# Performance work log

Measured on AMD Instinct MI355X. Metric: run time of the kernel, lower is better.

Reference implementation:

```python
import jax, jax.numpy as jnp
import numpy as np
from jax import lax

EPS = 1e-5  # BatchNorm eps (torch default)

def _up2_bilinear_ac(x):
    # bilinear upsample x2, align_corners=True; x: [B,C,H,W]
    B, C, H, W = x.shape
    def axis_interp(n_in, n_out):
        pos = jnp.arange(n_out, dtype=jnp.float32) * ((n_in - 1) / (n_out - 1))
        i0 = jnp.floor(pos).astype(jnp.int32)
        i1 = jnp.minimum(i0 + 1, n_in - 1)
        w = (pos - i0.astype(jnp.float32)).astype(x.dtype)
        return i0, i1, w
    i0, i1, wh = axis_interp(H, 2 * H)
    x = x[:, :, i0, :] * (1.0 - wh)[None, None, :, None] + x[:, :, i1, :] * wh[None, None, :, None]
    j0, j1, ww = axis_interp(W, 2 * W)
    x = x[:, :, :, j0] * (1.0 - ww) + x[:, :, :, j1] * ww
    return x

def setup_inputs() -> dict:
    key = jax.random.key(0)
    ks = jax.random.split(key, 8)
    B, Cin, Cout, H, W = 8, 64, 32, 128, 128
    att, K = 16, 2  # attention_channel = max(int(64*0.0625),16)=16; kernel_num=2
    n = lambda k, s, sc: jax.random.normal(k, s, jnp.float32) * sc
    return {
        'x': n(ks[0], (B, Cin, H, W), 1.0),
        'fc_w': n(ks[1], (att, Cin), 0.1),
        'bn_a_gamma': jnp.ones((att,), jnp.float32), 'bn_a_beta': jnp.zeros((att,), jnp.float32),
        'bn_a_mean': jnp.zeros((att,), jnp.float32), 'bn_a_var': jnp.ones((att,), jnp.float32),
        'ch_w': n(ks[2], (Cin, att), 0.1), 'ch_b': jnp.zeros((Cin,), jnp.float32),
        'fil_w': n(ks[3], (Cout, att), 0.1), 'fil_b': jnp.zeros((Cout,), jnp.float32),
        'sp_w': n(ks[4], (9, att), 0.1), 'sp_b': jnp.zeros((9,), jnp.float32),
        'k_w': n(ks[5], (K, att), 0.1), 'k_b': jnp.zeros((K,), jnp.float32),
        'weight': n(ks[6], (K, Cout, Cin, 3, 3), 0.05),
        'bn_gamma': jnp.ones((Cout,), jnp.float32), 'bn_beta': jnp.zeros((Cout,), jnp.float32),
        'bn_mean': jnp.zeros((Cout,), jnp.float32), 'bn_var': jnp.ones((Cout,), jnp.float32),
    }

def reference(x, fc_w, bn_a_gamma, bn_a_beta, bn_a_mean, bn_a_var,
              ch_w, ch_b, fil_w, fil_b, sp_w, sp_b, k_w, k_b,
              weight, bn_gamma, bn_beta, bn_mean, bn_var):
    x = _up2_bilinear_ac(x)
    B, Cin, H, W = x.shape
    K, Cout = weight.shape[0], weight.shape[1]
    # --- ODConv attention branch (on GAP features) ---
    g = x.mean(axis=(2, 3))                                    # [B,Cin]
    h = g @ fc_w.T                                             # [B,att]
    h = (h - bn_a_mean) / jnp.sqrt(bn_a_var + EPS) * bn_a_gamma + bn_a_beta
    h = jax.nn.relu(h)
    ch_att = jax.nn.sigmoid(h @ ch_w.T + ch_b)                 # [B,Cin]
    fil_att = jax.nn.sigmoid(h @ fil_w.T + fil_b)              # [B,Cout]
    sp_att = jax.nn.sigmoid(h @ sp_w.T + sp_b).reshape(B, 1, 1, 1, 3, 3)
    k_att = jax.nn.softmax(h @ k_w.T + k_b, axis=1).reshape(B, K, 1, 1, 1, 1)
    # per-sample aggregated filters: [B,Cout,Cin,3,3]
    agg_w = jnp.sum(k_att * sp_att * weight[None], axis=1)
    # --- dynamic conv (per-sample filter), channel-attended input ---
    x = x * ch_att[:, :, None, None]
    def conv1(xi, wi):
        return lax.conv_general_dilated(xi[None], wi, (1, 1), [(1, 1), (1, 1)],
                                        dimension_numbers=('NCHW', 'OIHW', 'NCHW'))[0]
    y = jax.vmap(conv1)(x, agg_w)                              # [B,Cout,H,W]
    y = y * fil_att[:, :, None, None]
    # --- BatchNorm2d (inference) + GELU (exact erf) ---
    y = (y - bn_mean[:, None, None]) / jnp.sqrt(bn_var[:, None, None] + EPS)
    y = y * bn_gamma[:, None, None] + bn_beta[:, None, None]
    return jax.nn.gelu(y, approximate=False)
```

## Files before the change

kernel.cpp:

```cpp
#include <hip/hip_runtime.h>
#include <hip/hip_bf16.h>

#define EPSBN 1e-5f

typedef short short8 __attribute__((ext_vector_type(8)));
typedef float f32x16 __attribute__((ext_vector_type(16)));

static __device__ __forceinline__ unsigned short f2u(float f){
  __hip_bfloat16 h = __float2bfloat16(f);
  union { __hip_bfloat16 h; unsigned short u; } c; c.h = h; return c.u;
}

#define WS_G     2048
#define WS_S     7168
#define WS_T     8192
#define WS_AGGB  16384
#define WS_XUP   327680

__global__ __launch_bounds__(256) void k_gap(const float* __restrict__ x, float* __restrict__ g){
  __shared__ float w[128];
  __shared__ float partial[4];
  int tid = threadIdx.x;
  if (tid < 128){
    int i = tid;
    float s = 0.f;
    int rstart = max(0, (int)floorf((float)(i-1)*(255.0f/127.0f)));
    #pragma unroll
    for (int k = 0; k < 8; ++k){
      int r = rstart + k;
      if (r <= 255){
        float pos = (float)r * (127.0f/255.0f);
        int i0 = (int)pos; float fr = pos - (float)i0; int i1 = min(i0+1,127);
        if (i0 == i) s += 1.0f - fr;
        if (i1 == i) s += fr;
      }
    }
    w[i] = s;
  }
  __syncthreads();
  const float4* xp = (const float4*)(x + ((size_t)blockIdx.x << 14));
  float s = 0.f;
  for (int gi = tid; gi < 4096; gi += 256){
    int i = gi >> 5, j4 = (gi & 31) * 4;
    float4 v = xp[gi];
    s += (v.x*w[j4] + v.y*w[j4+1] + v.z*w[j4+2] + v.w*w[j4+3]) * w[i];
  }
  for (int off = 32; off > 0; off >>= 1) s += __shfl_down(s, off, 64);
  if ((tid & 63) == 0) partial[tid >> 6] = s;
  __syncthreads();
  if (tid == 0) g[blockIdx.x] = (partial[0]+partial[1]+partial[2]+partial[3]) * (1.0f/65536.0f);
}

__global__ __launch_bounds__(256) void k_aggw(const float* __restrict__ g,
                      const float* __restrict__ fc_w,
                      const float* __restrict__ bga, const float* __restrict__ bba,
                      const float* __restrict__ bma, const float* __restrict__ bva,
                      const float* __restrict__ ch_w, const float* __restrict__ ch_b,
                      const float* __restrict__ fil_w, const float* __restrict__ fil_b,
                      const float* __restrict__ sp_w, const float* __restrict__ sp_b,
                      const float* __restrict__ k_w, const float* __restrict__ k_b,
                      const float* __restrict__ bn_g, const float* __restrict__ bn_b,
                      const float* __restrict__ bn_m, const float* __restrict__ bn_v,
                      const float* __restrict__ weight,
                      unsigned short* __restrict__ aggb,
                      float* __restrict__ sS, float* __restrict__ tT)
{
  __shared__ float h[8][16];
  int tid = threadIdx.x;
  if (tid < 128){
    int b = tid >> 4, a = tid & 15;
    float acc = 0.f;
    for (int c = 0; c < 64; ++c) acc += g[b*64+c] * fc_w[a*64+c];
    float v = (acc - bma[a]) * rsqrtf(bva[a] + EPSBN) * bga[a] + bba[a];
    h[b][a] = fmaxf(v, 0.f);
  }
  __syncthreads();

  int idx = blockIdx.x*256 + tid;
  int ci_l = idx & 31;
  int o    = (idx >> 5) & 31;
  int s    = (idx >> 10) % 9;
  int t2   = (idx >> 10) / 9;
  int cc   = t2 & 1, b = t2 >> 1;
  int ci   = cc*32 + ci_l;

  const float* hb = h[b];
  float zc = ch_b[ci], zs = sp_b[s];
  float z0 = k_b[0],  z1 = k_b[1];
  #pragma unroll
  for (int a = 0; a < 16; ++a){
    float hv = hb[a];
    zc += hv*ch_w[ci*16+a];
    zs += hv*sp_w[s*16+a];
    z0 += hv*k_w[a];
    z1 += hv*k_w[16+a];
  }
  float chv = 1.f/(1.f+expf(-zc));
  float spv = 1.f/(1.f+expf(-zs));
  float m = fmaxf(z0,z1);
  float e0 = expf(z0-m), e1 = expf(z1-m), inv = 1.f/(e0+e1);
  float ka0 = e0*inv, ka1 = e1*inv;
  float w0 = weight[(o*64+ci)*9+s];
  float w1 = weight[((32+o)*64+ci)*9+s];
  aggb[idx] = f2u(chv*spv*(ka0*w0 + ka1*w1));

  if (blockIdx.x == 0){
    int bb = tid >> 5, oo = tid & 31;
    float z = fil_b[oo];
    #pragma unroll
    for (int a = 0; a < 16; ++a) z += h[bb][a]*fil_w[oo*16+a];
    float f = 1.f/(1.f+expf(-z));
    float invs = rsqrtf(bn_v[oo] + EPSBN);
    sS[tid] = f * bn_g[oo] * invs;
    if (bb == 0) tT[oo] = bn_b[oo] - bn_m[oo]*bn_g[oo]*invs;
  }
}

__global__ __launch_bounds__(256) void k_up(const float* __restrict__ x,
                                            unsigned int* __restrict__ xup32)
{
  __shared__ float xin[16*798];
  int tid = threadIdx.x;
  int bi  = blockIdx.x;
  int strip = bi & 31, h16 = (bi >> 5) & 3, b = bi >> 7;
  int r0 = strip * 8;
  int i0b = (int)((float)r0 * (127.0f/255.0f));

  for (int e = tid; e < 12288; e += 256){
    int ir = e >> 11, rem = e & 2047, ci = rem >> 7, j = rem & 127;
    int row = min(i0b + ir, 127);
    xin[ci*798 + ir*133 + j] = x[(((size_t)(b*64 + h16*16 + ci)) << 14) + (row << 7) + j];
  }
  __syncthreads();

  int ci2 = tid & 7, cbase = tid >> 3;
  int j0t[8], j1t[8]; float wwt[8];
  #pragma unroll
  for (int jj = 0; jj < 8; ++jj){
    int c = cbase + 32*jj;
    float pos = (float)c * (127.0f/255.0f);
    int j0 = (int)pos;
    j0t[jj] = j0; j1t[jj] = min(j0+1,127); wwt[jj] = pos - (float)j0;
  }
  const float* base0 = &xin[(ci2*2+0)*798];
  const float* base1 = &xin[(ci2*2+1)*798];
  size_t plane32 = ((size_t)(b*4 + h16)) << 19;

  for (int rr = 0; rr < 8; ++rr){
    int r = r0 + rr;
    float posr = (float)r * (127.0f/255.0f);
    int i0 = (int)posr; float wh = posr - (float)i0;
    int ir0 = (i0 - i0b)*133, ir1 = (min(i0+1,127) - i0b)*133;
    #pragma unroll
    for (int jj = 0; jj < 8; ++jj){
      int c = cbase + 32*jj;
      int j0 = j0t[jj], j1 = j1t[jj]; float ww = wwt[jj];
      float v00 = base0[ir0+j0], v01 = base0[ir0+j1];
      float v10 = base0[ir1+j0], v11 = base0[ir1+j1];
      float a0 = v00 + (v01-v00)*ww;
      float a1 = v10 + (v11-v10)*ww;
      float r0v = a0 + (a1-a0)*wh;
      float u00 = base1[ir0+j0], u01 = base1[ir0+j1];
      float u10 = base1[ir1+j0], u11 = base1[ir1+j1];
      float b0 = u00 + (u01-u00)*ww;
      float b1 = u10 + (u11-u10)*ww;
      float r1v = b0 + (b1-b0)*wh;
      unsigned pack = (unsigned)f2u(r0v) | (((unsigned)f2u(r1v)) << 16);
      xup32[plane32 + (size_t)(r*256 + c)*8 + ci2] = pack;
    }
  }
}

#define XT_STRIDE 40
__global__ __launch_bounds__(256) void k_conv(const unsigned short* __restrict__ xup,
                                              const unsigned short* __restrict__ aggb,
                                              const float* __restrict__ sS,
                                              const float* __restrict__ tT,
                                              float* __restrict__ out)
{
  __shared__ unsigned short xt[18*18*XT_STRIDE];
  __shared__ float sSs[32], tTs[32];

  int tid = threadIdx.x;
  int bi  = blockIdx.x;
  int b   = bi >> 8, t = bi & 255;
  int p0  = (t >> 4) * 16, q0 = (t & 15) * 16;
  int lane = tid & 63, wv = tid >> 6;
  if (tid < 32){ sSs[tid] = sS[b*32+tid]; tTs[tid] = tT[tid]; }

  int ldsoff[6], pmoff[6]; bool val[6];
  int cnt = (tid < 16) ? 6 : 5;
  for (int k = 0; k < cnt; ++k){
    int e = tid + (k << 8);
    int rr = e / 72; int rem = e - rr*72;
    int qq = rem >> 2; int k2 = (rem >> 1) & 1; int kq = rem & 1;
    int gr = p0 - 1 + rr, gq = q0 - 1 + qq;
    val[k]    = ((unsigned)gr < 256u) && ((unsigned)gq < 256u);
    ldsoff[k] = (rr*18+qq)*XT_STRIDE + k2*16 + kq*8;
    pmoff[k]  = (k2 << 20) + (gr*256+gq)*16 + kq*8;
  }

  f32x16 acc[2];
  #pragma unroll
  for (int i = 0; i < 16; ++i){ acc[0][i] = 0.f; acc[1][i] = 0.f; }

  int n  = lane & 31;
  int kq = lane >> 5;

  for (int cc = 0; cc < 2; ++cc){
    if (cc) __syncthreads();
    const unsigned short* xb = xup + (((size_t)(b*4 + 2*cc)) << 20);
    for (int k = 0; k < cnt; ++k){
      short8 v = {0,0,0,0,0,0,0,0};
      if (val[k]) v = *(const short8*)&xb[pmoff[k]];
      *(short8*)&xt[ldsoff[k]] = v;
    }
    __syncthreads();

    const unsigned short* ab = aggb + (((size_t)(b*2+cc))*9*32 + n)*32 + kq*8;

    #pragma unroll
    for (int s = 0; s < 9; ++s){
      const int ky = s / 3, kx = s % 3;
      const unsigned short* ap = ab + s*1024;
      short8 av0 = *(const short8*)&ap[0];
      short8 av1 = *(const short8*)&ap[16];
      #pragma unroll
      for (int tt = 0; tt < 2; ++tt){
        int lr = 2*(2*wv + tt) + (n >> 4);
        int rr = lr + ky;
        int qq = (n & 15) + kx;
        const unsigned short* xrow = &xt[(rr*18+qq)*XT_STRIDE + kq*8];
        short8 bv0 = *(const short8*)&xrow[0];
        short8 bv1 = *(const short8*)&xrow[16];
        acc[tt] = __builtin_amdgcn_mfma_f32_32x32x16_bf16(av0, bv0, acc[tt], 0, 0, 0);
        acc[tt] = __builtin_amdgcn_mfma_f32_32x32x16_bf16(av1, bv1, acc[tt], 0, 0, 0);
      }
    }
  }

  #pragma unroll
  for (int tt = 0; tt < 2; ++tt){
    int lr = 2*(2*wv + tt) + (n >> 4);
    int p = p0 + lr, q = q0 + (n & 15);
    #pragma unroll
    for (int r = 0; r < 16; ++r){
      int o = (r & 3) + 8*(r >> 2) + 4*kq;
      float valv = acc[tt][r]*sSs[o] + tTs[o];
      float gl  = 0.5f*valv*(1.f + erff(valv*0.70710678118f));
      out[(((size_t)(b*32+o)) << 16) + (p << 8) + q] = gl;
    }
  }
}

extern "C" void kernel_launch(void* const* d_in, const int* in_sizes, int n_in,
                              void* d_out, int out_size, void* d_ws, size_t ws_size,
                              hipStream_t stream)
{
  const float* x     = (const float*)d_in[0];
  const float* fc_w  = (const float*)d_in[1];
  const float* bga   = (const float*)d_in[2];
  const float* bba   = (const float*)d_in[3];
  const float* bma   = (const float*)d_in[4];
  const float* bva   = (const float*)d_in[5];
  const float* ch_w  = (const float*)d_in[6];
  const float* ch_b  = (const float*)d_in[7];
  const float* fil_w = (const float*)d_in[8];
  const float* fil_b = (const float*)d_in[9];
  const float* sp_w  = (const float*)d_in[10];
  const float* sp_b  = (const float*)d_in[11];
  const float* k_w   = (const float*)d_in[12];
  const float* k_b   = (const float*)d_in[13];
  const float* weight= (const float*)d_in[14];
  const float* bn_g  = (const float*)d_in[15];
  const float* bn_b  = (const float*)d_in[16];
  const float* bn_m  = (const float*)d_in[17];
  const float* bn_v  = (const float*)d_in[18];

  char* ws = (char*)d_ws;
  float* g   = (float*)(ws + WS_G);
  float* sS  = (float*)(ws + WS_S);
  float* tT  = (float*)(ws + WS_T);
  unsigned short* aggb = (unsigned short*)(ws + WS_AGGB);
  unsigned short* xup  = (unsigned short*)(ws + WS_XUP);
  float* out = (float*)d_out;

  hipLaunchKernelGGL(k_gap,  dim3(512),  dim3(256), 0, stream, x, g);
  hipLaunchKernelGGL(k_aggw, dim3(576),  dim3(256), 0, stream, g, fc_w, bga, bba, bma, bva,
                     ch_w, ch_b, fil_w, fil_b, sp_w, sp_b, k_w, k_b,
                     bn_g, bn_b, bn_m, bn_v, weight, aggb, sS, tT);
  hipLaunchKernelGGL(k_up,   dim3(1024), dim3(256), 0, stream, x, (unsigned int*)xup);
  hipLaunchKernelGGL(k_conv, dim3(2048), dim3(256), 0, stream, xup, aggb, sS, tT, out);
}
```

Baseline: 201.3 us.

## Fuse GAP into upsample kernel and prefetch second channel chunk in conv

The global-average-pool reduction moves into the upsample kernel: each block reuses its staged input rows to compute partial weighted sums and adds them into g with atomics, after a memset. This removes a separate full read of x and one kernel launch. The conv kernel now prefetches the second channel-half tile into registers while the first half computes, and software-pipelines the weight fragment loads across filter taps. The cost is atomic float accumulation, which makes summation order nondeterministic, plus higher register pressure.

Result: faster. 191.0 us (-5.1%).

```diff
diff --git a/kernel.cpp b/kernel.cpp
--- a/kernel.cpp
+++ b/kernel.cpp
@@ -17,10 +17,18 @@
 #define WS_AGGB  16384
 #define WS_XUP   327680
 
-__global__ __launch_bounds__(256) void k_gap(const float* __restrict__ x, float* __restrict__ g){
+__global__ __launch_bounds__(256) void k_up(const float* __restrict__ x,
+                                            unsigned int* __restrict__ xup32,
+                                            float* __restrict__ g)
+{
+  __shared__ float xin[16*798];
   __shared__ float w[128];
-  __shared__ float partial[4];
   int tid = threadIdx.x;
+  int bi  = blockIdx.x;
+  int strip = bi & 31, h16 = (bi >> 5) & 3, b = bi >> 7;
+  int r0 = strip * 8;
+  int i0b = (int)((float)r0 * (127.0f/255.0f));
+
   if (tid < 128){
     int i = tid;
     float s = 0.f;
@@ -37,18 +45,70 @@
     }
     w[i] = s;
   }
-  __syncthreads();
-  const float4* xp = (const float4*)(x + ((size_t)blockIdx.x << 14));
-  float s = 0.f;
-  for (int gi = tid; gi < 4096; gi += 256){
-    int i = gi >> 5, j4 = (gi & 31) * 4;
-    float4 v = xp[gi];
-    s += (v.x*w[j4] + v.y*w[j4+1] + v.z*w[j4+2] + v.w*w[j4+3]) * w[i];
-  }
-  for (int off = 32; off > 0; off >>= 1) s += __shfl_down(s, off, 64);
-  if ((tid & 63) == 0) partial[tid >> 6] = s;
-  __syncthreads();
-  if (tid == 0) g[blockIdx.x] = (partial[0]+partial[1]+partial[2]+partial[3]) * (1.0f/65536.0f);
+  for (int e = tid; e < 12288; e += 256){
+    int ir = e >> 11, rem = e & 2047, ci = rem >> 7, j = rem & 127;
+    int row = min(i0b + ir, 127);
+    xin[ci*798 + ir*133 + j] = x[(((size_t)(b*64 + h16*16 + ci)) << 14) + (row << 7) + j];
+  }
+  __syncthreads();
+
+  {
+    int ci_l = tid >> 4, kk = tid & 15;
+    float s = 0.f;
+    const float* base = &xin[ci_l*798];
+    #pragma unroll
+    for (int row = 0; row < 4; ++row){
+      int grow = 4*strip + row;
+      int ir = grow - i0b;
+      const float* rp = base + ir*133 + kk*8;
+      float ss = 0.f;
+      #pragma unroll
+      for (int j = 0; j < 8; ++j) ss += rp[j]*w[kk*8+j];
+      s += w[grow]*ss;
+    }
+    s += __shfl_down(s, 8, 16);
+    s += __shfl_down(s, 4, 16);
+    s += __shfl_down(s, 2, 16);
+    s += __shfl_down(s, 1, 16);
+    if (kk == 0) atomicAdd(&g[b*64 + h16*16 + ci_l], s*(1.0f/65536.0f));
+  }
+
+  int ci2 = tid & 7, cbase = tid >> 3;
+  int j0t[8], j1t[8]; float wwt[8];
+  #pragma unroll
+  for (int jj = 0; jj < 8; ++jj){
+    int c = cbase + 32*jj;
+    float pos = (float)c * (127.0f/255.0f);
+    int j0 = (int)pos;
+    j0t[jj] = j0; j1t[jj] = min(j0+1,127); wwt[jj] = pos - (float)j0;
+  }
+  const float* base0 = &xin[(ci2*2+0)*798];
+  const float* base1 = &xin[(ci2*2+1)*798];
+  size_t plane32 = ((size_t)(b*4 + h16)) << 19;
+
+  for (int rr = 0; rr < 8; ++rr){
+    int r = r0 + rr;
+    float posr = (float)r * (127.0f/255.0f);
+    int i0 = (int)posr; float wh = posr - (float)i0;
+    int ir0 = (i0 - i0b)*133, ir1 = (min(i0+1,127) - i0b)*133;
+    #pragma unroll
+    for (int jj = 0; jj < 8; ++jj){
+      int c = cbase + 32*jj;
+      int j0 = j0t[jj], j1 = j1t[jj]; float ww = wwt[jj];
+      float v00 = base0[ir0+j0], v01 = base0[ir0+j1];
+      float v10 = base0[ir1+j0], v11 = base0[ir1+j1];
+      float a0 = v00 + (v01-v00)*ww;
+      float a1 = v10 + (v11-v10)*ww;
+      float r0v = a0 + (a1-a0)*wh;
+      float u00 = base1[ir0+j0], u01 = base1[ir0+j1];
+      float u10 = base1[ir1+j0], u11 = base1[ir1+j1];
+      float b0 = u00 + (u01-u00)*ww;
+      float b1 = u10 + (u11-u10)*ww;
+      float r1v = b0 + (b1-b0)*wh;
+      unsigned pack = (unsigned)f2u(r0v) | (((unsigned)f2u(r1v)) << 16);
+      xup32[plane32 + (size_t)(r*256 + c)*8 + ci2] = pack;
+    }
+  }
 }
 
 __global__ __launch_bounds__(256) void k_aggw(const float* __restrict__ g,
@@ -116,62 +176,18 @@
   }
 }
 
-__global__ __launch_bounds__(256) void k_up(const float* __restrict__ x,
-                                            unsigned int* __restrict__ xup32)
-{
-  __shared__ float xin[16*798];
-  int tid = threadIdx.x;
-  int bi  = blockIdx.x;
-  int strip = bi & 31, h16 = (bi >> 5) & 3, b = bi >> 7;
-  int r0 = strip * 8;
-  int i0b = (int)((float)r0 * (127.0f/255.0f));
-
-  for (int e = tid; e < 12288; e += 256){
-    int ir = e >> 11, rem = e & 2047, ci = rem >> 7, j = rem & 127;
-    int row = min(i0b + ir, 127);
-    xin[ci*798 + ir*133 + j] = x[(((size_t)(b*64 + h16*16 + ci)) << 14) + (row << 7) + j];
-  }
-  __syncthreads();
-
-  int ci2 = tid & 7, cbase = tid >> 3;
-  int j0t[8], j1t[8]; float wwt[8];
-  #pragma unroll
-  for (int jj = 0; jj < 8; ++jj){
-    int c = cbase + 32*jj;
-    float pos = (float)c * (127.0f/255.0f);
-    int j0 = (int)pos;
-    j0t[jj] = j0; j1t[jj] = min(j0+1,127); wwt[jj] = pos - (float)j0;
-  }
-  const float* base0 = &xin[(ci2*2+0)*798];
-  const float* base1 = &xin[(ci2*2+1)*798];
-  size_t plane32 = ((size_t)(b*4 + h16)) << 19;
-
-  for (int rr = 0; rr < 8; ++rr){
-    int r = r0 + rr;
-    float posr = (float)r * (127.0f/255.0f);
-    int i0 = (int)posr; float wh = posr - (float)i0;
-    int ir0 = (i0 - i0b)*133, ir1 = (min(i0+1,127) - i0b)*133;
-    #pragma unroll
-    for (int jj = 0; jj < 8; ++jj){
-      int c = cbase + 32*jj;
-      int j0 = j0t[jj], j1 = j1t[jj]; float ww = wwt[jj];
-      float v00 = base0[ir0+j0], v01 = base0[ir0+j1];
-      float v10 = base0[ir1+j0], v11 = base0[ir1+j1];
-      float a0 = v00 + (v01-v00)*ww;
-      float a1 = v10 + (v11-v10)*ww;
-      float r0v = a0 + (a1-a0)*wh;
-      float u00 = base1[ir0+j0], u01 = base1[ir0+j1];
-      float u10 = base1[ir1+j0], u11 = base1[ir1+j1];
-      float b0 = u00 + (u01-u00)*ww;
-      float b1 = u10 + (u11-u10)*ww;
-      float r1v = b0 + (b1-b0)*wh;
-      unsigned pack = (unsigned)f2u(r0v) | (((unsigned)f2u(r1v)) << 16);
-      xup32[plane32 + (size_t)(r*256 + c)*8 + ci2] = pack;
-    }
-  }
-}
-
 #define XT_STRIDE 40
+
+static __device__ __forceinline__ void xdesc(int e, int p0, int q0,
+                                             int& ldso, int& pmo, bool& v){
+  int rr = e / 72; int rem = e - rr*72;
+  int qq = rem >> 2; int k2 = (rem >> 1) & 1; int kqe = rem & 1;
+  int gr = p0 - 1 + rr, gq = q0 - 1 + qq;
+  v    = ((unsigned)gr < 256u) && ((unsigned)gq < 256u);
+  ldso = (rr*18+qq)*XT_STRIDE + k2*16 + kqe*8;
+  pmo  = (k2 << 20) + (gr*256+gq)*16 + kqe*8;
+}
+
 __global__ __launch_bounds__(256) void k_conv(const unsigned short* __restrict__ xup,
                                               const unsigned short* __restrict__ aggb,
                                               const float* __restrict__ sS,
@@ -188,61 +204,83 @@
   int lane = tid & 63, wv = tid >> 6;
   if (tid < 32){ sSs[tid] = sS[b*32+tid]; tTs[tid] = tT[tid]; }
 
-  int ldsoff[6], pmoff[6]; bool val[6];
-  int cnt = (tid < 16) ? 6 : 5;
-  for (int k = 0; k < cnt; ++k){
-    int e = tid + (k << 8);
-    int rr = e / 72; int rem = e - rr*72;
-    int qq = rem >> 2; int k2 = (rem >> 1) & 1; int kq = rem & 1;
-    int gr = p0 - 1 + rr, gq = q0 - 1 + qq;
-    val[k]    = ((unsigned)gr < 256u) && ((unsigned)gq < 256u);
-    ldsoff[k] = (rr*18+qq)*XT_STRIDE + k2*16 + kq*8;
-    pmoff[k]  = (k2 << 20) + (gr*256+gq)*16 + kq*8;
-  }
-
   f32x16 acc[2];
   #pragma unroll
   for (int i = 0; i < 16; ++i){ acc[0][i] = 0.f; acc[1][i] = 0.f; }
 
   int n  = lane & 31;
   int kq = lane >> 5;
-
-  for (int cc = 0; cc < 2; ++cc){
-    if (cc) __syncthreads();
-    const unsigned short* xb = xup + (((size_t)(b*4 + 2*cc)) << 20);
-    for (int k = 0; k < cnt; ++k){
-      short8 v = {0,0,0,0,0,0,0,0};
-      if (val[k]) v = *(const short8*)&xb[pmoff[k]];
-      *(short8*)&xt[ldsoff[k]] = v;
-    }
-    __syncthreads();
-
-    const unsigned short* ab = aggb + (((size_t)(b*2+cc))*9*32 + n)*32 + kq*8;
-
+  int lr0 = 2*(2*wv + 0) + (n >> 4);
+  int lr1 = 2*(2*wv + 1) + (n >> 4);
+  int qb  = n & 15;
+
+  const unsigned short* xb0 = xup + (((size_t)(b*4 + 0)) << 20);
+  const unsigned short* xb1 = xup + (((size_t)(b*4 + 2)) << 20);
+  const short8 zero8 = {0,0,0,0,0,0,0,0};
+
+  #pragma unroll
+  for (int k = 0; k < 6; ++k){
+    int e = tid + (k << 8); if (e >= 1296) e -= 1296;
+    int ldso, pmo; bool v;
+    xdesc(e, p0, q0, ldso, pmo, v);
+    short8 vv = zero8;
+    if (v) vv = *(const short8*)&xb0[pmo];
+    *(short8*)&xt[ldso] = vv;
+  }
+  short8 pre[6];
+  #pragma unroll
+  for (int k = 0; k < 6; ++k){
+    int e = tid + (k << 8); if (e >= 1296) e -= 1296;
+    int ldso, pmo; bool v;
+    xdesc(e, p0, q0, ldso, pmo, v);
+    pre[k] = zero8;
+    if (v) pre[k] = *(const short8*)&xb1[pmo];
+  }
+  __syncthreads();
+
+  auto kloop = [&](const unsigned short* ab){
+    short8 a0 = *(const short8*)&ab[0];
+    short8 a1 = *(const short8*)&ab[16];
     #pragma unroll
     for (int s = 0; s < 9; ++s){
-      const int ky = s / 3, kx = s % 3;
-      const unsigned short* ap = ab + s*1024;
-      short8 av0 = *(const short8*)&ap[0];
-      short8 av1 = *(const short8*)&ap[16];
-      #pragma unroll
-      for (int tt = 0; tt < 2; ++tt){
-        int lr = 2*(2*wv + tt) + (n >> 4);
-        int rr = lr + ky;
-        int qq = (n & 15) + kx;
-        const unsigned short* xrow = &xt[(rr*18+qq)*XT_STRIDE + kq*8];
+      int sn = (s < 8) ? s+1 : 8;
+      short8 na0 = *(const short8*)&ab[sn*1024];
+      short8 na1 = *(const short8*)&ab[sn*1024+16];
+      const int ky = s/3, kx = s%3;
+      {
+        const unsigned short* xrow = &xt[((lr0+ky)*18 + qb+kx)*XT_STRIDE + kq*8];
         short8 bv0 = *(const short8*)&xrow[0];
         short8 bv1 = *(const short8*)&xrow[16];
-        acc[tt] = __builtin_amdgcn_mfma_f32_32x32x16_bf16(av0, bv0, acc[tt], 0, 0, 0);
-        acc[tt] = __builtin_amdgcn_mfma_f32_32x32x16_bf16(av1, bv1, acc[tt], 0, 0, 0);
+        acc[0] = __builtin_amdgcn_mfma_f32_32x32x16_bf16(a0, bv0, acc[0], 0, 0, 0);
+        acc[0] = __builtin_amdgcn_mfma_f32_32x32x16_bf16(a1, bv1, acc[0], 0, 0, 0);
       }
-    }
-  }
+      {
+        const unsigned short* xrow = &xt[((lr1+ky)*18 + qb+kx)*XT_STRIDE + kq*8];
+        short8 bv0 = *(const short8*)&xrow[0];
+        short8 bv1 = *(const short8*)&xrow[16];
+        acc[1] = __builtin_amdgcn_mfma_f32_32x32x16_bf16(a0, bv0, acc[1], 0, 0, 0);
+        acc[1] = __builtin_amdgcn_mfma_f32_32x32x16_bf16(a1, bv1, acc[1], 0, 0, 0);
+      }
+      a0 = na0; a1 = na1;
+    }
+  };
+
+  kloop(aggb + (size_t)(b*2+0)*9216 + n*32 + kq*8);
+  __syncthreads();
+  #pragma unroll
+  for (int k = 0; k < 6; ++k){
+    int e = tid + (k << 8); if (e >= 1296) e -= 1296;
+    int ldso, pmo; bool v;
+    xdesc(e, p0, q0, ldso, pmo, v);
+    *(short8*)&xt[ldso] = pre[k];
+  }
+  __syncthreads();
+  kloop(aggb + (size_t)(b*2+1)*9216 + n*32 + kq*8);
 
   #pragma unroll
   for (int tt = 0; tt < 2; ++tt){
-    int lr = 2*(2*wv + tt) + (n >> 4);
-    int p = p0 + lr, q = q0 + (n & 15);
+    int lr = (tt == 0) ? lr0 : lr1;
+    int p = p0 + lr, q = q0 + qb;
     #pragma unroll
     for (int r = 0; r < 16; ++r){
       int o = (r & 3) + 8*(r >> 2) + 4*kq;
@@ -285,10 +323,10 @@
   unsigned short* xup  = (unsigned short*)(ws + WS_XUP);
   float* out = (float*)d_out;
 
-  hipLaunchKernelGGL(k_gap,  dim3(512),  dim3(256), 0, stream, x, g);
+  hipMemsetAsync(g, 0, 512*sizeof(float), stream);
+  hipLaunchKernelGGL(k_up,   dim3(1024), dim3(256), 0, stream, x, (unsigned int*)xup, g);
   hipLaunchKernelGGL(k_aggw, dim3(576),  dim3(256), 0, stream, g, fc_w, bga, bba, bma, bva,
                      ch_w, ch_b, fil_w, fil_b, sp_w, sp_b, k_w, k_b,
                      bn_g, bn_b, bn_m, bn_v, weight, aggb, sS, tT);
-  hipLaunchKernelGGL(k_up,   dim3(1024), dim3(256), 0, stream, x, (unsigned int*)xup);
   hipLaunchKernelGGL(k_conv, dim3(2048), dim3(256), 0, stream, xup, aggb, sS, tT, out);
 }
```
